# Performance work log

Measured on AMD Instinct MI355X. Metric: run time of the kernel, lower is better.

The kernel has to match this reference:

```python
import jax, jax.numpy as jnp
import numpy as np

EPS_LN = 1e-6


def _ln(x):
    m = jnp.mean(x, axis=-1, keepdims=True)
    v = jnp.mean((x - m) ** 2, axis=-1, keepdims=True)
    return (x - m) * jax.lax.rsqrt(v + EPS_LN)


def _rope(q, cos, sin):
    # q: [B,S,H,D]; cos/sin: [S, D//2]; rotate interleaved pairs
    q2 = q.reshape(q.shape[:-1] + (-1, 2))
    a, b = q2[..., 0], q2[..., 1]
    c = cos[None, :, None, :]
    s = sin[None, :, None, :]
    return jnp.stack([a * c - b * s, a * s + b * c], axis=-1).reshape(q.shape)


def _attn(q, k, v):
    # q:[B,Sq,H,D] k,v:[B,Sk,H,D] -> [B,Sq,H,D]; flash default scale 1/sqrt(D)
    D = q.shape[-1]
    scores = jnp.einsum('bqhd,bkhd->bhqk', q, k) / jnp.sqrt(jnp.asarray(D, q.dtype))
    p = jax.nn.softmax(scores, axis=-1)
    return jnp.einsum('bhqk,bkhd->bqhd', p, v)


def setup_inputs() -> dict:
    key = jax.random.key(0)
    C, H, S, T, B = 2048, 16, 1024, 256, 4
    Dh = C // H
    F = int(C * 4)
    L, Ly = B * S, B * T
    ks = jax.random.split(key, 24)

    def w(k, shape):
        return (jax.random.normal(k, shape, dtype=jnp.float32) * 0.02)

    # RoPE angle table: positions 0..S-1 with standard inverse frequencies
    inv_freq = 1.0 / (10000.0 ** (np.arange(0, Dh, 2, dtype=np.float32) / Dh))
    freqs = jnp.asarray(np.arange(S, dtype=np.float32)[:, None] * inv_freq[None, :])

    inp = {
        'x': jax.random.normal(ks[0], (L, C), dtype=jnp.float32),
        'y': jax.random.normal(ks[1], (Ly, C), dtype=jnp.float32),
        't': jax.random.normal(ks[2], (L, 6 * C), dtype=jnp.float32),
        'freqs': freqs,
        'scale_shift_table': jax.random.normal(ks[3], (6, C), dtype=jnp.float32) / (C ** 0.5),
        'Wq_s': w(ks[4], (C, C)), 'bq_s': jnp.zeros((C,), jnp.float32),
        'Wk_s': w(ks[5], (C, C)), 'bk_s': jnp.zeros((C,), jnp.float32),
        'Wv_s': w(ks[6], (C, C)), 'bv_s': jnp.zeros((C,), jnp.float32),
        'Wo_s': w(ks[7], (C, C)), 'bo_s': jnp.zeros((C,), jnp.float32),
        'Wq_c': w(ks[8], (C, C)), 'bq_c': jnp.zeros((C,), jnp.float32),
        'Wk_c': w(ks[9], (C, C)), 'bk_c': jnp.zeros((C,), jnp.float32),
        'Wv_c': w(ks[10], (C, C)), 'bv_c': jnp.zeros((C,), jnp.float32),
        'Wo_c': w(ks[11], (C, C)), 'bo_c': jnp.zeros((C,), jnp.float32),
        'W_fc1': w(ks[12], (F, C)), 'b_fc1': jnp.zeros((F,), jnp.float32),
        'W_fc2': w(ks[13], (C, F)), 'b_fc2': jnp.zeros((C,), jnp.float32),
        'seq_len': S,
        'txt_len': T,
    }
    return inp


def reference(x, y, t, freqs, scale_shift_table,
              Wq_s, bq_s, Wk_s, bk_s, Wv_s, bv_s, Wo_s, bo_s,
              Wq_c, bq_c, Wk_c, bk_c, Wv_c, bv_c, Wo_c, bo_c,
              W_fc1, b_fc1, W_fc2, b_fc2, seq_len, txt_len):
    L, C = x.shape
    Dh = 2 * freqs.shape[1]
    H = C // Dh
    B = L // seq_len
    cos, sin = jnp.cos(freqs), jnp.sin(freqs)

    # per-token AdaLN params (B here == total tokens in torch code)
    mods = scale_shift_table[None] + t.reshape(L, 6, C)
    shift_msa, scale_msa, gate_msa, shift_mlp, scale_mlp, gate_mlp = (
        mods[:, i, :] for i in range(6))

    # ---- self attention (AdaLN modulate + RoPE) ----
    xm = _ln(x) * (1.0 + scale_msa) + shift_msa
    q = (xm @ Wq_s.T + bq_s).reshape(B, seq_len, H, Dh)
    k = (xm @ Wk_s.T + bk_s).reshape(B, seq_len, H, Dh)
    v = (xm @ Wv_s.T + bv_s).reshape(B, seq_len, H, Dh)
    q = _rope(q, cos, sin)
    k = _rope(k, cos, sin)
    a = _attn(q, k, v).reshape(L, C)
    x = x + gate_msa * (a @ Wo_s.T + bo_s)

    # ---- cross attention (no norm/modulation/gate, no RoPE) ----
    q = (x @ Wq_c.T + bq_c).reshape(B, seq_len, H, Dh)
    k = (y @ Wk_c.T + bk_c).reshape(B, txt_len, H, Dh)
    v = (y @ Wv_c.T + bv_c).reshape(B, txt_len, H, Dh)
    a = _attn(q, k, v).reshape(L, C)
    x = x + (a @ Wo_c.T + bo_c)

    # ---- MLP with AdaLN modulate + gate ----
    xm = _ln(x) * (1.0 + scale_mlp) + shift_mlp
    h = jax.nn.gelu(xm @ W_fc1.T + b_fc1, approximate=True)
    x = x + gate_mlp * (h @ W_fc2.T + b_fc2)
    return x
```

## Files before the change

kernel.cpp:

```cpp
#include <hip/hip_runtime.h>
#include <stdint.h>

#define C_DIM 2048
#define H_NUM 16
#define DH    128
#define S_LEN 1024
#define T_LEN 256
#define B_SZ  4
#define L_ROWS 4096
#define LY_ROWS 1024
#define F_DIM 8192

typedef __attribute__((ext_vector_type(4))) float f32x4;
typedef __attribute__((ext_vector_type(8))) __bf16 bf16x8;
typedef __attribute__((ext_vector_type(4))) unsigned short us4;
typedef __attribute__((ext_vector_type(8))) unsigned short us8;
typedef unsigned short u16;

__device__ __forceinline__ u16 f2bf(float f) {
  union { float f; uint32_t u; } v; v.f = f;
  uint32_t r = v.u + 0x7FFFu + ((v.u >> 16) & 1u);
  return (u16)(r >> 16);
}
__device__ __forceinline__ float bf2f(u16 h) {
  union { uint32_t u; float f; } v; v.u = ((uint32_t)h) << 16;
  return v.f;
}

typedef __attribute__((address_space(1))) void gvoid;
typedef __attribute__((address_space(3))) void lvoid;
__device__ __forceinline__ void gl_lds16(const void* g, void* l) {
  __builtin_amdgcn_global_load_lds((gvoid*)g, (lvoid*)l, 16, 0, 0);
}

template<int N> __device__ __forceinline__ void wait_vmcnt() {
  if constexpr (N == 0) asm volatile("s_waitcnt vmcnt(0)" ::: "memory");
  else if constexpr (N == 4) asm volatile("s_waitcnt vmcnt(4)" ::: "memory");
  else if constexpr (N == 5) asm volatile("s_waitcnt vmcnt(5)" ::: "memory");
  else if constexpr (N == 6) asm volatile("s_waitcnt vmcnt(6)" ::: "memory");
}
__device__ __forceinline__ void barrier_raw() {
  asm volatile("s_barrier" ::: "memory");
}
__device__ __forceinline__ void lgkm0_pin() {
  asm volatile("s_waitcnt lgkmcnt(0)" ::: "memory");
  __builtin_amdgcn_sched_barrier(0);
}

__device__ __forceinline__ float gelu_fast(float val) {
  float z = 0.7978845608f * (val + 0.044715f * val * val * val);
  float e = __expf(2.f * z);
  float th = 1.f - 2.f / (e + 1.f);
  return 0.5f * val * (1.f + th);
}

__global__ void k_cvt(const float* __restrict__ src, u16* __restrict__ dst, int n) {
  int i = (blockIdx.x * blockDim.x + threadIdx.x) * 4;
  int stride = gridDim.x * blockDim.x * 4;
  for (; i < n; i += stride) {
    float4 v = *(const float4*)(src + i);
    us4 o;
    o[0] = f2bf(v.x); o[1] = f2bf(v.y); o[2] = f2bf(v.z); o[3] = f2bf(v.w);
    *(us4*)(dst + i) = o;
  }
}

__global__ void k_cvt8(const float* __restrict__ s0, const float* __restrict__ s1,
                       const float* __restrict__ s2, const float* __restrict__ s3,
                       const float* __restrict__ s4, const float* __restrict__ s5,
                       const float* __restrict__ s6, const float* __restrict__ s7,
                       u16* __restrict__ dst) {
  const int PER = C_DIM * C_DIM;
  int i = (blockIdx.x * blockDim.x + threadIdx.x) * 4;
  int stride = gridDim.x * blockDim.x * 4;
  int total = PER * 8;
  for (; i < total; i += stride) {
    int t = i >> 22;
    const float* s;
    switch (t) {
      case 0: s = s0; break; case 1: s = s1; break;
      case 2: s = s2; break; case 3: s = s3; break;
      case 4: s = s4; break; case 5: s = s5; break;
      case 6: s = s6; break; default: s = s7; break;
    }
    float4 v = *(const float4*)(s + (i & (PER - 1)));
    us4 o;
    o[0] = f2bf(v.x); o[1] = f2bf(v.y); o[2] = f2bf(v.z); o[3] = f2bf(v.w);
    *(us4*)(dst + i) = o;
  }
}

__global__ void k_cvt2(const float* __restrict__ s0, const float* __restrict__ s1,
                       u16* __restrict__ dst) {
  const int PER = F_DIM * C_DIM;
  int i = (blockIdx.x * blockDim.x + threadIdx.x) * 4;
  int stride = gridDim.x * blockDim.x * 4;
  int total = PER * 2;
  for (; i < total; i += stride) {
    const float* s = (i >> 24) ? s1 : s0;
    float4 v = *(const float4*)(s + (i & (PER - 1)));
    us4 o;
    o[0] = f2bf(v.x); o[1] = f2bf(v.y); o[2] = f2bf(v.z); o[3] = f2bf(v.w);
    *(us4*)(dst + i) = o;
  }
}

template<int INBF>
__global__ __launch_bounds__(256)
void k_modln(const void* __restrict__ xin, const float* __restrict__ t,
             const float* __restrict__ tab, u16* __restrict__ out,
             int scale_idx, int shift_idx) {
  int row = blockIdx.x;
  int tid = threadIdx.x;
  int c0 = tid * 8;
  float v[8];
  if constexpr (INBF) {
    us8 a = *(const us8*)((const u16*)xin + (size_t)row * C_DIM + c0);
#pragma unroll
    for (int j = 0; j < 8; ++j) v[j] = bf2f(a[j]);
  } else {
    const float* xr = (const float*)xin + (size_t)row * C_DIM;
    float4 a = *(const float4*)(xr + c0);
    float4 b = *(const float4*)(xr + c0 + 4);
    v[0] = a.x; v[1] = a.y; v[2] = a.z; v[3] = a.w;
    v[4] = b.x; v[5] = b.y; v[6] = b.z; v[7] = b.w;
  }
  float s = 0.f, ss = 0.f;
#pragma unroll
  for (int j = 0; j < 8; ++j) { s += v[j]; ss += v[j] * v[j]; }
#pragma unroll
  for (int m = 1; m < 64; m <<= 1) { s += __shfl_xor(s, m); ss += __shfl_xor(ss, m); }
  __shared__ float red[8];
  int wid = tid >> 6;
  if ((tid & 63) == 0) { red[wid * 2] = s; red[wid * 2 + 1] = ss; }
  __syncthreads();
  s  = red[0] + red[2] + red[4] + red[6];
  ss = red[1] + red[3] + red[5] + red[7];
  float mean = s * (1.f / C_DIM);
  float var  = ss * (1.f / C_DIM) - mean * mean;
  float rstd = rsqrtf(var + 1e-6f);
  const float* trow = t + (size_t)row * (6 * C_DIM);
  const float* tsc = trow + scale_idx * C_DIM + c0;
  const float* tsh = trow + shift_idx * C_DIM + c0;
  const float* gsc = tab + scale_idx * C_DIM + c0;
  const float* gsh = tab + shift_idx * C_DIM + c0;
  us8 o;
#pragma unroll
  for (int j = 0; j < 8; ++j) {
    float scv = 1.f + gsc[j] + tsc[j];
    float shv = gsh[j] + tsh[j];
    o[j] = f2bf((v[j] - mean) * rstd * scv + shv);
  }
  *(us8*)(out + (size_t)row * C_DIM + c0) = o;
}

template<int EPI>
__global__ __launch_bounds__(512, 2)
void k_gemm5(const u16* __restrict__ A, const u16* __restrict__ W,
             const float* __restrict__ bias0, const float* __restrict__ bias1,
             const float* __restrict__ bias2,
             u16* __restrict__ o0, u16* __restrict__ o1, u16* __restrict__ o2,
             int sec_shift, int out_ld,
             int M, int N, int K, int lda, int ldw, int nbx) {
  __shared__ __align__(16) u16 lds[65536];

  int tid = threadIdx.x;
  int nwg = gridDim.x;
  int q8 = nwg >> 3, r8 = nwg & 7;
  int xcd = blockIdx.x & 7, local = blockIdx.x >> 3;
  int wgid = (xcd < r8 ? xcd * (q8 + 1) : r8 * (q8 + 1) + (xcd - r8) * q8) + local;
  int bx = wgid % nbx, by = wgid / nbx;
  int m0 = by * 256, n0 = bx * 256;

  int wid = tid >> 6, lane = tid & 63;
  int wm = wid >> 2, wn = wid & 3;
  int lr = lane & 15, lg = lane >> 4;
  int xorslot = lr & 7;
  int bcol = (wn & 1) * 64;

  int srow = tid >> 3;
  int scol = ((tid ^ (tid >> 3)) & 7) * 8;

  auto stA = [&](int buf, int h, int kt) {
    u16* dst = lds + (buf * 2 + h) * 8192 + tid * 8;
#pragma unroll
    for (int call = 0; call < 2; ++call) {
      int grow = m0 + h * 128 + call * 64 + srow;
      gl_lds16(A + (size_t)grow * lda + kt * 64 + scol, dst + call * 4096);
    }
  };
  auto stB = [&](int buf, int h, int kt) {
    u16* dst = lds + 32768 + (buf * 2 + h) * 8192 + tid * 8;
#pragma unroll
    for (int call = 0; call < 2; ++call) {
      int grow = n0 + h * 128 + call * 64 + srow;
      gl_lds16(W + (size_t)grow * ldw + kt * 64 + scol, dst + call * 4096);
    }
  };

  f32x4 zero4 = {0.f, 0.f, 0.f, 0.f};
  f32x4 acc[8][4];
#pragma unroll
  for (int m = 0; m < 8; ++m)
#pragma unroll
    for (int n = 0; n < 4; ++n) acc[m][n] = zero4;

  int NT = K >> 6, NJ = NT >> 1;
  stA(0, 0, 0); stA(0, 1, 0); stB(0, 0, 0); stB(0, 1, 0);
  stB(1, 0, 1); stA(1, 0, 1);
  wait_vmcnt<4>();
  barrier_raw();

  for (int j = 0; j < NJ; ++j) {
    bool nlast = (j + 1 < NJ);
    int t1 = 2 * j + 1, t2 = 2 * j + 2, t3 = 2 * j + 3;
#pragma unroll
    for (int buf = 0; buf < 2; ++buf) {
      const u16* Ah = lds + (buf * 2 + wm) * 8192;
      const u16* Bh = lds + 32768 + (buf * 2 + (wn >> 1)) * 8192;
      bf16x8 aR[4][2], b0[2][2], b1[2][2];

#pragma unroll
      for (int m = 0; m < 4; ++m) {
        int r = m * 16 + lr;
#pragma unroll
        for (int kk = 0; kk < 2; ++kk)
          aR[m][kk] = *(const bf16x8*)(Ah + r * 64 + (((kk << 2) | lg) ^ xorslot) * 8);
      }
#pragma unroll
      for (int n = 0; n < 2; ++n) {
        int r = bcol + n * 16 + lr;
#pragma unroll
        for (int kk = 0; kk < 2; ++kk)
          b0[n][kk] = *(const bf16x8*)(Bh + r * 64 + (((kk << 2) | lg) ^ xorslot) * 8);
      }
      if (buf == 0) stA(1, 1, t1);
      else if (nlast) stA(0, 1, t2);
      barrier_raw();
      lgkm0_pin();
      __builtin_amdgcn_s_setprio(1);
#pragma unroll
      for (int kk = 0; kk < 2; ++kk)
#pragma unroll
        for (int m = 0; m < 4; ++m)
#pragma unroll
          for (int n = 0; n < 2; ++n)
            acc[m][n] = __builtin_amdgcn_mfma_f32_16x16x32_bf16(aR[m][kk], b0[n][kk], acc[m][n], 0, 0, 0);
      __builtin_amdgcn_s_setprio(0);
      barrier_raw();

#pragma unroll
      for (int n = 0; n < 2; ++n) {
        int r = bcol + 32 + n * 16 + lr;
#pragma unroll
        for (int kk = 0; kk < 2; ++kk)
          b1[n][kk] = *(const bf16x8*)(Bh + r * 64 + (((kk << 2) | lg) ^ xorslot) * 8);
      }
      if (buf == 0) stB(1, 1, t1);
      else if (nlast) stB(0, 1, t2);
      barrier_raw();
      lgkm0_pin();
      __builtin_amdgcn_s_setprio(1);
#pragma unroll
      for (int kk = 0; kk < 2; ++kk)
#pragma unroll
        for (int m = 0; m < 4; ++m)
#pragma unroll
          for (int n = 0; n < 2; ++n)
            acc[m][2 + n] = __builtin_amdgcn_mfma_f32_16x16x32_bf16(aR[m][kk], b1[n][kk], acc[m][2 + n], 0, 0, 0);
      __builtin_amdgcn_s_setprio(0);
      barrier_raw();

#pragma unroll
      for (int m = 0; m < 4; ++m) {
        int r = 64 + m * 16 + lr;
#pragma unroll
        for (int kk = 0; kk < 2; ++kk)
          aR[m][kk] = *(const bf16x8*)(Ah + r * 64 + (((kk << 2) | lg) ^ xorslot) * 8);
      }
      if (nlast) { if (buf == 0) stB(0, 0, t2); else stB(1, 0, t3); }
      barrier_raw();
      lgkm0_pin();
      __builtin_amdgcn_s_setprio(1);
#pragma unroll
      for (int kk = 0; kk < 2; ++kk)
#pragma unroll
        for (int m = 0; m < 4; ++m)
#pragma unroll
          for (int n = 0; n < 2; ++n)
            acc[4 + m][2 + n] = __builtin_amdgcn_mfma_f32_16x16x32_bf16(aR[m][kk], b1[n][kk], acc[4 + m][2 + n], 0, 0, 0);
      __builtin_amdgcn_s_setprio(0);
      barrier_raw();

      if (nlast) { if (buf == 0) stA(0, 0, t2); else stA(1, 0, t3); }
      barrier_raw();
      __builtin_amdgcn_s_setprio(1);
#pragma unroll
      for (int kk = 0; kk < 2; ++kk)
#pragma unroll
        for (int m = 0; m < 4; ++m)
#pragma unroll
          for (int n = 0; n < 2; ++n)
            acc[4 + m][n] = __builtin_amdgcn_mfma_f32_16x16x32_bf16(aR[m][kk], b0[n][kk], acc[4 + m][n], 0, 0, 0);
      __builtin_amdgcn_s_setprio(0);
      if (nlast) wait_vmcnt<4>(); else wait_vmcnt<0>();
      barrier_raw();
    }
  }

#pragma unroll
  for (int mf = 0; mf < 8; ++mf) {
    int row0 = m0 + wm * 128 + mf * 16 + lg * 4;
#pragma unroll
    for (int nf = 0; nf < 4; ++nf) {
      int col = n0 + wn * 64 + nf * 16 + lr;
      if constexpr (EPI == 0) {
        int sec = col >> sec_shift;
        const float* bp = sec == 0 ? bias0 : (sec == 1 ? bias1 : bias2);
        u16* op = sec == 0 ? o0 : (sec == 1 ? o1 : o2);
        int cs = col & ((1 << sec_shift) - 1);
        float bv = bp[cs];
#pragma unroll
        for (int r = 0; r < 4; ++r)
          op[(size_t)(row0 + r) * out_ld + cs] = f2bf(acc[mf][nf][r] + bv);
      } else {
        float bv = bias0[col];
#pragma unroll
        for (int r = 0; r < 4; ++r)
          o0[(size_t)(row0 + r) * out_ld + col] = f2bf(gelu_fast(acc[mf][nf][r] + bv));
      }
    }
  }
}

template<int BM, int EPI>
__global__ __launch_bounds__(512, 2)
void k_gemm3(const u16* __restrict__ A, const u16* __restrict__ W,
             const float* __restrict__ bias0, const float* __restrict__ bias1,
             const float* __restrict__ bias2,
             u16* __restrict__ o0, u16* __restrict__ o1, u16* __restrict__ o2,
             int sec_shift, int out_ld,
             float* __restrict__ outF, const float* __restrict__ resid,
             const float* __restrict__ gate_t, const float* __restrict__ gate_tab,
             int M, int N, int K, int lda, int ldw, int nbx) {
  constexpr int HTA = (BM / 2) * 64;
  constexpr int HTB = 128 * 64;
  constexpr int ACALLS = BM / 128;
  constexpr int QM = BM / 64;
  constexpr int MFR = BM / 32;
  constexpr int VMN = 4 + ACALLS;
  constexpr int BOFF = 4 * HTA;
  __shared__ __align__(16) u16 lds[BOFF + 4 * HTB];

  int tid = threadIdx.x;
  int nwg = gridDim.x;
  int q8 = nwg >> 3, r8 = nwg & 7;
  int xcd = blockIdx.x & 7, local = blockIdx.x >> 3;
  int wgid = (xcd < r8 ? xcd * (q8 + 1) : r8 * (q8 + 1) + (xcd - r8) * q8) + local;
  int bx = wgid % nbx, by = wgid / nbx;
  int m0 = by * BM, n0 = bx * 256;

  int wid = tid >> 6, lane = tid & 63;
  int wm = wid >> 2, wn = wid & 3;
  int lr = lane & 15, lg = lane >> 4;
  int xorslot = lr & 7;
  int bcol = (wn & 1) * 64;

  int srow = tid >> 3;
  int scol = ((tid ^ (tid >> 3)) & 7) * 8;

  auto stA = [&](int h, int kt2) {
    int pt = kt2 & 1;
    u16* dst = lds + (pt * 2 + h) * HTA + tid * 8;
#pragma unroll
    for (int call = 0; call < ACALLS; ++call) {
      int grow = m0 + h * (BM / 2) + call * 64 + srow;
      gl_lds16(A + (size_t)grow * lda + kt2 * 64 + scol, dst + call * 4096);
    }
  };
  auto stB = [&](int h, int kt2) {
    int pt = kt2 & 1;
    u16* dst = lds + BOFF + (pt * 2 + h) * HTB + tid * 8;
#pragma unroll
    for (int call = 0; call < 2; ++call) {
      int grow = n0 + h * 128 + call * 64 + srow;
      gl_lds16(W + (size_t)grow * ldw + kt2 * 64 + scol, dst + call * 4096);
    }
  };

  f32x4 zero4 = {0.f, 0.f, 0.f, 0.f};
  f32x4 acc[MFR][4];
#pragma unroll
  for (int m = 0; m < MFR; ++m)
#pragma unroll
    for (int n = 0; n < 4; ++n) acc[m][n] = zero4;

  int NT2 = K >> 6;
  stA(0, 0); stA(1, 0); stB(0, 0); stB(1, 0);
  stB(0, 1); stB(1, 1); stA(0, 1);
  wait_vmcnt<VMN>();
  barrier_raw();

  for (int kt = 0; kt < NT2; ++kt) {
    int p = kt & 1;
    const u16* Ah = lds + (p * 2 + wm) * HTA;
    const u16* Bh = lds + BOFF + (p * 2 + (wn >> 1)) * HTB;
    bf16x8 aR[QM][2], bR0[2][2], bR1[2][2];
    bool st1 = (kt + 1) < NT2, st2 = (kt + 2) < NT2;

#pragma unroll
    for (int m = 0; m < QM; ++m) {
      int r = m * 16 + lr;
#pragma unroll
      for (int kk = 0; kk < 2; ++kk)
        aR[m][kk] = *(const bf16x8*)(Ah + r * 64 + (((kk << 2) | lg) ^ xorslot) * 8);
    }
#pragma unroll
    for (int n = 0; n < 2; ++n) {
      int r = bcol + n * 16 + lr;
#pragma unroll
      for (int kk = 0; kk < 2; ++kk)
        bR0[n][kk] = *(const bf16x8*)(Bh + r * 64 + (((kk << 2) | lg) ^ xorslot) * 8);
    }
    if (st1) stA(1, kt + 1);
    lgkm0_pin();
    __builtin_amdgcn_s_setprio(1);
#pragma unroll
    for (int kk = 0; kk < 2; ++kk)
#pragma unroll
      for (int m = 0; m < QM; ++m)
#pragma unroll
        for (int n = 0; n < 2; ++n)
          acc[m][n] = __builtin_amdgcn_mfma_f32_16x16x32_bf16(aR[m][kk], bR0[n][kk], acc[m][n], 0, 0, 0);
    __builtin_amdgcn_s_setprio(0);
    barrier_raw();

#pragma unroll
    for (int n = 0; n < 2; ++n) {
      int r = bcol + 32 + n * 16 + lr;
#pragma unroll
      for (int kk = 0; kk < 2; ++kk)
        bR1[n][kk] = *(const bf16x8*)(Bh + r * 64 + (((kk << 2) | lg) ^ xorslot) * 8);
    }
    lgkm0_pin();
    __builtin_amdgcn_s_setprio(1);
#pragma unroll
    for (int kk = 0; kk < 2; ++kk)
#pragma unroll
      for (int m = 0; m < QM; ++m)
#pragma unroll
        for (int n = 0; n < 2; ++n)
          acc[m][2 + n] = __builtin_amdgcn_mfma_f32_16x16x32_bf16(aR[m][kk], bR1[n][kk], acc[m][2 + n], 0, 0, 0);
    __builtin_amdgcn_s_setprio(0);
    barrier_raw();

#pragma unroll
    for (int m = 0; m < QM; ++m) {
      int r = (BM / 4) + m * 16 + lr;
#pragma unroll
      for (int kk = 0; kk < 2; ++kk)
        aR[m][kk] = *(const bf16x8*)(Ah + r * 64 + (((kk << 2) | lg) ^ xorslot) * 8);
    }
    if (st2) { stB(0, kt + 2); stB(1, kt + 2); }
    lgkm0_pin();
    __builtin_amdgcn_s_setprio(1);
#pragma unroll
    for (int kk = 0; kk < 2; ++kk)
#pragma unroll
      for (int m = 0; m < QM; ++m)
#pragma unroll
        for (int n = 0; n < 2; ++n)
          acc[QM + m][2 + n] = __builtin_amdgcn_mfma_f32_16x16x32_bf16(aR[m][kk], bR1[n][kk], acc[QM + m][2 + n], 0, 0, 0);
    __builtin_amdgcn_s_setprio(0);
    barrier_raw();

    if (st2) stA(0, kt + 2);
    __builtin_amdgcn_s_setprio(1);
#pragma unroll
    for (int kk = 0; kk < 2; ++kk)
#pragma unroll
      for (int m = 0; m < QM; ++m)
#pragma unroll
        for (int n = 0; n < 2; ++n)
          acc[QM + m][n] = __builtin_amdgcn_mfma_f32_16x16x32_bf16(aR[m][kk], bR0[n][kk], acc[QM + m][n], 0, 0, 0);
    __builtin_amdgcn_s_setprio(0);
    if (st2) wait_vmcnt<VMN>(); else wait_vmcnt<0>();
    barrier_raw();
  }

#pragma unroll
  for (int mf = 0; mf < MFR; ++mf) {
    int row0 = m0 + wm * (BM / 2) + mf * 16 + lg * 4;
#pragma unroll
    for (int nf = 0; nf < 4; ++nf) {
      int col = n0 + wn * 64 + nf * 16 + lr;
      if constexpr (EPI == 0) {
        int sec = col >> sec_shift;
        const float* bp = sec == 0 ? bias0 : (sec == 1 ? bias1 : bias2);
        u16* op = sec == 0 ? o0 : (sec == 1 ? o1 : o2);
        int cs = col & ((1 << sec_shift) - 1);
        float bv = bp[cs];
#pragma unroll
        for (int r = 0; r < 4; ++r)
          op[(size_t)(row0 + r) * out_ld + cs] = f2bf(acc[mf][nf][r] + bv);
      } else if constexpr (EPI == 6) {
        float bv = bias0[col];
        float gt = gate_tab[col];
#pragma unroll
        for (int r = 0; r < 4; ++r) {
          int row = row0 + r;
          size_t idx = (size_t)row * N + col;
          float g = gt + gate_t[(size_t)row * (6 * C_DIM) + col];
          o0[idx] = f2bf(resid[idx] + g * (acc[mf][nf][r] + bv));
        }
      } else if constexpr (EPI == 7) {
        float bv = bias0[col];
#pragma unroll
        for (int r = 0; r < 4; ++r) {
          size_t idx = (size_t)(row0 + r) * N + col;
          o0[idx] = f2bf(bf2f(o0[idx]) + acc[mf][nf][r] + bv);
        }
      } else {
        float bv = bias0[col];
        float gt = gate_tab[col];
#pragma unroll
        for (int r = 0; r < 4; ++r) {
          int row = row0 + r;
          size_t idx = (size_t)row * N + col;
          float g = gt + gate_t[(size_t)row * (6 * C_DIM) + col];
          outF[idx] = bf2f(((const u16*)o1)[idx]) + g * (acc[mf][nf][r] + bv);
        }
      }
    }
  }
}

__global__ void k_rope(u16* __restrict__ q, u16* __restrict__ k,
                       const float* __restrict__ freqs) {
  int idx = blockIdx.x * blockDim.x + threadIdx.x;
  int total = L_ROWS * C_DIM / 8;
  for (; idx < total; idx += gridDim.x * blockDim.x) {
    int e = idx * 8;
    int row = e >> 11;
    int col = e & (C_DIM - 1);
    int s = row & (S_LEN - 1);
    int i0 = (col & (DH - 1)) >> 1;
    float4 fr = *(const float4*)(freqs + s * (DH / 2) + i0);
    float cs[4], sn[4];
    float fv[4] = {fr.x, fr.y, fr.z, fr.w};
#pragma unroll
    for (int j = 0; j < 4; ++j) __sincosf(fv[j], &sn[j], &cs[j]);
    us8 qa = *(us8*)(q + e);
    us8 ka = *(us8*)(k + e);
#pragma unroll
    for (int p = 0; p < 4; ++p) {
      float a = bf2f(qa[2 * p]), b = bf2f(qa[2 * p + 1]);
      qa[2 * p]     = f2bf(a * cs[p] - b * sn[p]);
      qa[2 * p + 1] = f2bf(a * sn[p] + b * cs[p]);
      float a2 = bf2f(ka[2 * p]), b2 = bf2f(ka[2 * p + 1]);
      ka[2 * p]     = f2bf(a2 * cs[p] - b2 * sn[p]);
      ka[2 * p + 1] = f2bf(a2 * sn[p] + b2 * cs[p]);
    }
    *(us8*)(q + e) = qa;
    *(us8*)(k + e) = ka;
  }
}

__global__ void k_transpose_v(const u16* __restrict__ v, u16* __restrict__ vt, int Lkv) {
  __shared__ u16 tile[32][33];
  int bh = blockIdx.x, b = bh >> 4, h = bh & 15;
  int k0 = blockIdx.y * 32, d0 = blockIdx.z * 32;
  int tx = threadIdx.x, ty = threadIdx.y;
  const u16* src = v + (size_t)(b * Lkv) * C_DIM + h * DH;
#pragma unroll
  for (int j = 0; j < 32; j += 8)
    tile[ty + j][tx] = src[(size_t)(k0 + ty + j) * C_DIM + d0 + tx];
  __syncthreads();
  u16* dst = vt + (size_t)bh * DH * Lkv;
#pragma unroll
  for (int j = 0; j < 32; j += 8)
    dst[(size_t)(d0 + ty + j) * Lkv + k0 + tx] = tile[tx][ty + j];
}

__global__ __launch_bounds__(256)
void k_flash(const u16* __restrict__ Q, const u16* __restrict__ K,
             const u16* __restrict__ Vt, u16* __restrict__ O,
             int Lq, int Lkv, float scale2) {
  __shared__ __align__(16) u16 lK[64 * 128];
  __shared__ __align__(16) u16 lV[128 * 64];
  __shared__ __align__(16) u16 lP[4][16 * 72];
  int bh = blockIdx.x, b = bh >> 4, h = bh & 15;
  int tid = threadIdx.x, wid = tid >> 6, lane = tid & 63;
  int lr = lane & 15, lg = lane >> 4;
  int q0 = blockIdx.y * 64 + wid * 16;
  const u16* Qb = Q + ((size_t)(b * Lq) + q0) * C_DIM + h * DH;
  const u16* Kb = K + (size_t)(b * Lkv) * C_DIM + h * DH;
  const u16* Vb = Vt + (size_t)bh * DH * Lkv;

  bf16x8 qf[4];
#pragma unroll
  for (int ks = 0; ks < 4; ++ks)
    qf[ks] = *(const bf16x8*)(Qb + (size_t)lr * C_DIM + ks * 32 + lg * 8);

  f32x4 zero4 = {0.f, 0.f, 0.f, 0.f};
  f32x4 o[8];
#pragma unroll
  for (int n = 0; n < 8; ++n) o[n] = zero4;
  float mrow[4] = {-3.0e38f, -3.0e38f, -3.0e38f, -3.0e38f};
  float lrow[4] = {0.f, 0.f, 0.f, 0.f};

  int nsteps = Lkv >> 6;
  for (int kt = 0; kt < nsteps; ++kt) {
#pragma unroll
    for (int i = 0; i < 4; ++i) {
      int flat = i * 4096 + tid * 16;
      int key = flat >> 8, inner = flat & 255;
      int ksrc = inner ^ ((key & 7) << 4);
      gl_lds16((const char*)Kb + ((size_t)(kt * 64 + key) * C_DIM) * 2 + ksrc, (char*)lK + flat);
      int d = flat >> 7, keyb = flat & 127;
      int vsrc = keyb ^ ((d & 7) << 4);
      gl_lds16((const char*)Vb + ((size_t)d * Lkv) * 2 + kt * 128 + vsrc, (char*)lV + flat);
    }
    __syncthreads();

    f32x4 sc[4];
#pragma unroll
    for (int c = 0; c < 4; ++c) sc[c] = zero4;
#pragma unroll
    for (int c = 0; c < 4; ++c) {
      int key = c * 16 + lr;
#pragma unroll
      for (int ks = 0; ks < 4; ++ks) {
        int off = (ks * 64 + lg * 16) ^ ((key & 7) << 4);
        bf16x8 kf = *(const bf16x8*)((const char*)lK + key * 256 + off);
        sc[c] = __builtin_amdgcn_mfma_f32_16x16x32_bf16(qf[ks], kf, sc[c], 0, 0, 0);
      }
    }
#pragma unroll
    for (int r = 0; r < 4; ++r) {
      float s0 = sc[0][r] * scale2, s1 = sc[1][r] * scale2;
      float s2 = sc[2][r] * scale2, s3 = sc[3][r] * scale2;
      float mx = fmaxf(fmaxf(s0, s1), fmaxf(s2, s3));
#pragma unroll
      for (int m = 1; m < 16; m <<= 1) mx = fmaxf(mx, __shfl_xor(mx, m));
      float mnew = fmaxf(mrow[r], mx);
      float alpha = exp2f(mrow[r] - mnew);
      mrow[r] = mnew;
      float p0 = exp2f(s0 - mnew);
      float p1 = exp2f(s1 - mnew);
      float p2 = exp2f(s2 - mnew);
      float p3 = exp2f(s3 - mnew);
      float psum = p0 + p1 + p2 + p3;
#pragma unroll
      for (int m = 1; m < 16; m <<= 1) psum += __shfl_xor(psum, m);
      lrow[r] = lrow[r] * alpha + psum;
#pragma unroll
      for (int n = 0; n < 8; ++n) o[n][r] *= alpha;
      u16* pr = lP[wid] + (4 * lg + r) * 72;
      pr[lr]      = f2bf(p0);
      pr[16 + lr] = f2bf(p1);
      pr[32 + lr] = f2bf(p2);
      pr[48 + lr] = f2bf(p3);
    }
    asm volatile("s_waitcnt lgkmcnt(0)" ::: "memory");
    __builtin_amdgcn_sched_barrier(0);
#pragma unroll
    for (int half = 0; half < 2; ++half) {
      bf16x8 pf = *(const bf16x8*)(lP[wid] + lr * 72 + half * 32 + lg * 8);
#pragma unroll
      for (int n = 0; n < 8; ++n) {
        int d = n * 16 + lr;
        int off = (half * 64 + lg * 16) ^ ((d & 7) << 4);
        bf16x8 vf = *(const bf16x8*)((const char*)lV + d * 128 + off);
        o[n] = __builtin_amdgcn_mfma_f32_16x16x32_bf16(pf, vf, o[n], 0, 0, 0);
      }
    }
    __syncthreads();
  }

  u16* Ob = O + ((size_t)(b * Lq) + q0) * C_DIM + h * DH;
#pragma unroll
  for (int n = 0; n < 8; ++n) {
    int d = n * 16 + lr;
#pragma unroll
    for (int r = 0; r < 4; ++r) {
      int qr = 4 * lg + r;
      Ob[(size_t)qr * C_DIM + d] = f2bf(o[n][r] / lrow[r]);
    }
  }
}

extern "C" void kernel_launch(void* const* d_in, const int* in_sizes, int n_in,
                              void* d_out, int out_size, void* d_ws, size_t ws_size,
                              hipStream_t stream) {
  const float* x     = (const float*)d_in[0];
  const float* y     = (const float*)d_in[1];
  const float* t     = (const float*)d_in[2];
  const float* freqs = (const float*)d_in[3];
  const float* tab   = (const float*)d_in[4];
  const float* Wq_s = (const float*)d_in[5];
  const float* bq_s = (const float*)d_in[6];
  const float* Wk_s = (const float*)d_in[7];
  const float* bk_s = (const float*)d_in[8];
  const float* Wv_s = (const float*)d_in[9];
  const float* bv_s = (const float*)d_in[10];
  const float* Wo_s = (const float*)d_in[11];
  const float* bo_s = (const float*)d_in[12];
  const float* Wq_c = (const float*)d_in[13];
  const float* bq_c = (const float*)d_in[14];
  const float* Wk_c = (const float*)d_in[15];
  const float* bk_c = (const float*)d_in[16];
  const float* Wv_c = (const float*)d_in[17];
  const float* bv_c = (const float*)d_in[18];
  const float* Wo_c = (const float*)d_in[19];
  const float* bo_c = (const float*)d_in[20];
  const float* W_fc1 = (const float*)d_in[21];
  const float* b_fc1 = (const float*)d_in[22];
  const float* W_fc2 = (const float*)d_in[23];
  const float* b_fc2 = (const float*)d_in[24];

  const size_t SZ_CC  = (size_t)C_DIM * C_DIM * 2;
  const size_t SZ_FC  = (size_t)F_DIM * C_DIM * 2;
  const size_t SZ_LC  = (size_t)L_ROWS * C_DIM * 2;
  const size_t SZ_YC  = (size_t)LY_ROWS * C_DIM * 2;
  char* ws = (char*)d_ws;
  size_t off = 0;
  u16* wq_s = (u16*)(ws + off); off += SZ_CC;
  u16* wk_s = (u16*)(ws + off); off += SZ_CC;
  u16* wv_s = (u16*)(ws + off); off += SZ_CC;
  u16* wo_s = (u16*)(ws + off); off += SZ_CC;
  u16* wq_c = (u16*)(ws + off); off += SZ_CC;
  u16* wk_c = (u16*)(ws + off); off += SZ_CC;
  u16* wv_c = (u16*)(ws + off); off += SZ_CC;
  u16* wo_c = (u16*)(ws + off); off += SZ_CC;
  u16* wfc1 = (u16*)(ws + off); off += SZ_FC;
  u16* wfc2 = (u16*)(ws + off); off += SZ_FC;
  u16* ybf  = (u16*)(ws + off); off += SZ_YC;
  u16* xm   = (u16*)(ws + off); off += SZ_LC;
  u16* qb   = (u16*)(ws + off); off += SZ_LC;
  u16* kb   = (u16*)(ws + off); off += SZ_LC;
  u16* vb   = (u16*)(ws + off); off += SZ_LC;
  u16* ao   = (u16*)(ws + off); off += SZ_LC;
  u16* hbuf = qb;
  u16* x1bf = (u16*)(ws + off); off += SZ_LC;
  u16* kc   = (u16*)(ws + off); off += SZ_YC;
  u16* vc   = (u16*)(ws + off); off += SZ_YC;
  u16* vt   = (u16*)(ws + off); off += SZ_LC;
  u16* vtc  = (u16*)(ws + off); off += SZ_YC;
  if (ws_size < off) return;

  k_cvt8<<<4096, 256, 0, stream>>>(Wq_s, Wk_s, Wv_s, Wo_s, Wq_c, Wk_c, Wv_c, Wo_c, wq_s);
  k_cvt2<<<4096, 256, 0, stream>>>(W_fc1, W_fc2, wfc1);
  k_cvt<<<2048, 256, 0, stream>>>(y, ybf, LY_ROWS * C_DIM);

  const float ascale2 = 0.08838834764831845f * 1.44269504f;

  k_modln<0><<<L_ROWS, 256, 0, stream>>>(x, t, tab, xm, 1, 0);
  k_gemm3<128, 0><<<32 * 24, 512, 0, stream>>>(
      xm, wq_s, bq_s, bk_s, bv_s, qb, kb, vb, 11, C_DIM,
      nullptr, nullptr, nullptr, nullptr, L_ROWS, 6144, C_DIM, C_DIM, C_DIM, 24);
  k_rope<<<2048, 256, 0, stream>>>(qb, kb, freqs);
  k_transpose_v<<<dim3(B_SZ * H_NUM, S_LEN / 32, DH / 32), dim3(32, 8), 0, stream>>>(vb, vt, S_LEN);
  k_flash<<<dim3(B_SZ * H_NUM, S_LEN / 64), 256, 0, stream>>>(qb, kb, vt, ao, S_LEN, S_LEN, ascale2);
  k_gemm3<128, 6><<<32 * 8, 512, 0, stream>>>(
      ao, wo_s, bo_s, nullptr, nullptr, x1bf, nullptr, nullptr, 30, C_DIM,
      nullptr, x, t + 2 * C_DIM, tab + 2 * C_DIM, L_ROWS, C_DIM, C_DIM, C_DIM, C_DIM, 8);
  k_gemm3<128, 0><<<32 * 8, 512, 0, stream>>>(
      x1bf, wq_c, bq_c, nullptr, nullptr, qb, nullptr, nullptr, 30, C_DIM,
      nullptr, nullptr, nullptr, nullptr, L_ROWS, C_DIM, C_DIM, C_DIM, C_DIM, 8);
  k_gemm3<128, 0><<<8 * 16, 512, 0, stream>>>(
      ybf, wk_c, bk_c, bv_c, bv_c, kc, vc, vc, 11, C_DIM,
      nullptr, nullptr, nullptr, nullptr, LY_ROWS, 4096, C_DIM, C_DIM, C_DIM, 16);
  k_transpose_v<<<dim3(B_SZ * H_NUM, T_LEN / 32, DH / 32), dim3(32, 8), 0, stream>>>(vc, vtc, T_LEN);
  k_flash<<<dim3(B_SZ * H_NUM, S_LEN / 64), 256, 0, stream>>>(qb, kc, vtc, ao, S_LEN, T_LEN, ascale2);
  k_gemm3<128, 7><<<32 * 8, 512, 0, stream>>>(
      ao, wo_c, bo_c, nullptr, nullptr, x1bf, nullptr, nullptr, 30, C_DIM,
      nullptr, nullptr, nullptr, nullptr, L_ROWS, C_DIM, C_DIM, C_DIM, C_DIM, 8);
  k_modln<1><<<L_ROWS, 256, 0, stream>>>(x1bf, t, tab, xm, 4, 3);
  k_gemm5<1><<<16 * 32, 512, 0, stream>>>(
      xm, wfc1, b_fc1, nullptr, nullptr, hbuf, nullptr, nullptr, 30, F_DIM,
      L_ROWS, F_DIM, C_DIM, C_DIM, C_DIM, 32);
  k_gemm3<128, 8><<<32 * 8, 512, 0, stream>>>(
      hbuf, wfc2, b_fc2, nullptr, nullptr, nullptr, x1bf, nullptr, 30, C_DIM,
      (float*)d_out, nullptr, t + 5 * C_DIM, tab + 5 * C_DIM, L_ROWS, C_DIM, F_DIM, F_DIM, F_DIM, 8);
}
```

Measured before the change: 843.0 us.

## Fuse RoPE and V transpose into QKV projection GEMM epilogues

The self-attention QKV GEMM epilogue now applies RoPE to Q and K, pairing even and odd columns with a lane shuffle and computing sincos from the freqs table. It also writes V directly in the transposed per-head layout that flash attention expects. The cross-attention KV GEMM likewise writes V transposed, so the separate rope and transpose kernels and their extra global round trips are gone. The cost is heavier epilogues with per-element sincos and strided, poorly coalesced transposed stores. An unused multi-output path was also dropped from the FC1 GEMM.

Measured after the change: 835.2 us. No clear change (-0.9%).

```diff
diff --git a/kernel.cpp b/kernel.cpp
--- a/kernel.cpp
+++ b/kernel.cpp
@@ -157,10 +157,8 @@
 template<int EPI>
 __global__ __launch_bounds__(512, 2)
 void k_gemm5(const u16* __restrict__ A, const u16* __restrict__ W,
-             const float* __restrict__ bias0, const float* __restrict__ bias1,
-             const float* __restrict__ bias2,
-             u16* __restrict__ o0, u16* __restrict__ o1, u16* __restrict__ o2,
-             int sec_shift, int out_ld,
+             const float* __restrict__ bias0,
+             u16* __restrict__ o0, int out_ld,
              int M, int N, int K, int lda, int ldw, int nbx) {
   __shared__ __align__(16) u16 lds[65536];
 
@@ -314,21 +312,10 @@
 #pragma unroll
     for (int nf = 0; nf < 4; ++nf) {
       int col = n0 + wn * 64 + nf * 16 + lr;
-      if constexpr (EPI == 0) {
-        int sec = col >> sec_shift;
-        const float* bp = sec == 0 ? bias0 : (sec == 1 ? bias1 : bias2);
-        u16* op = sec == 0 ? o0 : (sec == 1 ? o1 : o2);
-        int cs = col & ((1 << sec_shift) - 1);
-        float bv = bp[cs];
-#pragma unroll
-        for (int r = 0; r < 4; ++r)
-          op[(size_t)(row0 + r) * out_ld + cs] = f2bf(acc[mf][nf][r] + bv);
-      } else {
-        float bv = bias0[col];
-#pragma unroll
-        for (int r = 0; r < 4; ++r)
-          o0[(size_t)(row0 + r) * out_ld + col] = f2bf(gelu_fast(acc[mf][nf][r] + bv));
-      }
+      float bv = bias0[col];
+#pragma unroll
+      for (int r = 0; r < 4; ++r)
+        o0[(size_t)(row0 + r) * out_ld + col] = f2bf(gelu_fast(acc[mf][nf][r] + bv));
     }
   }
 }
@@ -520,7 +507,7 @@
           size_t idx = (size_t)(row0 + r) * N + col;
           o0[idx] = f2bf(bf2f(o0[idx]) + acc[mf][nf][r] + bv);
         }
-      } else {
+      } else if constexpr (EPI == 8) {
         float bv = bias0[col];
         float gt = gate_tab[col];
 #pragma unroll
@@ -530,56 +517,57 @@
           float g = gt + gate_t[(size_t)row * (6 * C_DIM) + col];
           outF[idx] = bf2f(((const u16*)o1)[idx]) + g * (acc[mf][nf][r] + bv);
         }
+      } else if constexpr (EPI == 9) {
+        int sec = col >> 11;
+        int cs = col & 2047;
+        const float* bp = sec == 0 ? bias0 : (sec == 1 ? bias1 : bias2);
+        float bv = bp[cs];
+        if (sec < 2) {
+          u16* op = sec == 0 ? o0 : o1;
+          int i0 = (cs & (DH - 1)) >> 1;
+          bool even = (cs & 1) == 0;
+#pragma unroll
+          for (int r = 0; r < 4; ++r) {
+            float val = acc[mf][nf][r] + bv;
+            float pv = __shfl_xor(val, 1);
+            int sr = (row0 + r) & (S_LEN - 1);
+            float ang = gate_t[sr * (DH / 2) + i0];
+            float sn, csn;
+            __sincosf(ang, &sn, &csn);
+            float outv = even ? (val * csn - pv * sn) : (pv * sn + val * csn);
+            op[(size_t)(row0 + r) * out_ld + cs] = f2bf(outv);
+          }
+        } else {
+          int h = cs >> 7, d = cs & (DH - 1);
+#pragma unroll
+          for (int r = 0; r < 4; ++r) {
+            int row = row0 + r;
+            int b = row >> 10, kv = row & (S_LEN - 1);
+            o2[(((size_t)(b * H_NUM + h) * DH + d) << 10) + kv] =
+                f2bf(acc[mf][nf][r] + bv);
+          }
+        }
+      } else {
+        int sec = col >> 11;
+        int cs = col & 2047;
+        float bv = (sec == 0 ? bias0 : bias1)[cs];
+        if (sec == 0) {
+#pragma unroll
+          for (int r = 0; r < 4; ++r)
+            o0[(size_t)(row0 + r) * out_ld + cs] = f2bf(acc[mf][nf][r] + bv);
+        } else {
+          int h = cs >> 7, d = cs & (DH - 1);
+#pragma unroll
+          for (int r = 0; r < 4; ++r) {
+            int row = row0 + r;
+            int b = row >> 8, kv = row & (T_LEN - 1);
+            o1[(((size_t)(b * H_NUM + h) * DH + d) << 8) + kv] =
+                f2bf(acc[mf][nf][r] + bv);
+          }
+        }
       }
     }
   }
-}
-
-__global__ void k_rope(u16* __restrict__ q, u16* __restrict__ k,
-                       const float* __restrict__ freqs) {
-  int idx = blockIdx.x * blockDim.x + threadIdx.x;
-  int total = L_ROWS * C_DIM / 8;
-  for (; idx < total; idx += gridDim.x * blockDim.x) {
-    int e = idx * 8;
-    int row = e >> 11;
-    int col = e & (C_DIM - 1);
-    int s = row & (S_LEN - 1);
-    int i0 = (col & (DH - 1)) >> 1;
-    float4 fr = *(const float4*)(freqs + s * (DH / 2) + i0);
-    float cs[4], sn[4];
-    float fv[4] = {fr.x, fr.y, fr.z, fr.w};
-#pragma unroll
-    for (int j = 0; j < 4; ++j) __sincosf(fv[j], &sn[j], &cs[j]);
-    us8 qa = *(us8*)(q + e);
-    us8 ka = *(us8*)(k + e);
-#pragma unroll
-    for (int p = 0; p < 4; ++p) {
-      float a = bf2f(qa[2 * p]), b = bf2f(qa[2 * p + 1]);
-      qa[2 * p]     = f2bf(a * cs[p] - b * sn[p]);
-      qa[2 * p + 1] = f2bf(a * sn[p] + b * cs[p]);
-      float a2 = bf2f(ka[2 * p]), b2 = bf2f(ka[2 * p + 1]);
-      ka[2 * p]     = f2bf(a2 * cs[p] - b2 * sn[p]);
-      ka[2 * p + 1] = f2bf(a2 * sn[p] + b2 * cs[p]);
-    }
-    *(us8*)(q + e) = qa;
-    *(us8*)(k + e) = ka;
-  }
-}
-
-__global__ void k_transpose_v(const u16* __restrict__ v, u16* __restrict__ vt, int Lkv) {
-  __shared__ u16 tile[32][33];
-  int bh = blockIdx.x, b = bh >> 4, h = bh & 15;
-  int k0 = blockIdx.y * 32, d0 = blockIdx.z * 32;
-  int tx = threadIdx.x, ty = threadIdx.y;
-  const u16* src = v + (size_t)(b * Lkv) * C_DIM + h * DH;
-#pragma unroll
-  for (int j = 0; j < 32; j += 8)
-    tile[ty + j][tx] = src[(size_t)(k0 + ty + j) * C_DIM + d0 + tx];
-  __syncthreads();
-  u16* dst = vt + (size_t)bh * DH * Lkv;
-#pragma unroll
-  for (int j = 0; j < 32; j += 8)
-    dst[(size_t)(d0 + ty + j) * Lkv + k0 + tx] = tile[tx][ty + j];
 }
 
 __global__ __launch_bounds__(256)
@@ -748,6 +736,7 @@
   u16* vt   = (u16*)(ws + off); off += SZ_LC;
   u16* vtc  = (u16*)(ws + off); off += SZ_YC;
   if (ws_size < off) return;
+  (void)vb; (void)vc;
 
   k_cvt8<<<4096, 256, 0, stream>>>(Wq_s, Wk_s, Wv_s, Wo_s, Wq_c, Wk_c, Wv_c, Wo_c, wq_s);
   k_cvt2<<<4096, 256, 0, stream>>>(W_fc1, W_fc2, wfc1);
@@ -756,11 +745,9 @@
   const float ascale2 = 0.08838834764831845f * 1.44269504f;
 
   k_modln<0><<<L_ROWS, 256, 0, stream>>>(x, t, tab, xm, 1, 0);
-  k_gemm3<128, 0><<<32 * 24, 512, 0, stream>>>(
-      xm, wq_s, bq_s, bk_s, bv_s, qb, kb, vb, 11, C_DIM,
-      nullptr, nullptr, nullptr, nullptr, L_ROWS, 6144, C_DIM, C_DIM, C_DIM, 24);
-  k_rope<<<2048, 256, 0, stream>>>(qb, kb, freqs);
-  k_transpose_v<<<dim3(B_SZ * H_NUM, S_LEN / 32, DH / 32), dim3(32, 8), 0, stream>>>(vb, vt, S_LEN);
+  k_gemm3<128, 9><<<32 * 24, 512, 0, stream>>>(
+      xm, wq_s, bq_s, bk_s, bv_s, qb, kb, vt, 11, C_DIM,
+      nullptr, nullptr, freqs, nullptr, L_ROWS, 6144, C_DIM, C_DIM, C_DIM, 24);
   k_flash<<<dim3(B_SZ * H_NUM, S_LEN / 64), 256, 0, stream>>>(qb, kb, vt, ao, S_LEN, S_LEN, ascale2);
   k_gemm3<128, 6><<<32 * 8, 512, 0, stream>>>(
       ao, wo_s, bo_s, nullptr, nullptr, x1bf, nullptr, nullptr, 30, C_DIM,
@@ -768,18 +755,16 @@
   k_gemm3<128, 0><<<32 * 8, 512, 0, stream>>>(
       x1bf, wq_c, bq_c, nullptr, nullptr, qb, nullptr, nullptr, 30, C_DIM,
       nullptr, nullptr, nullptr, nullptr, L_ROWS, C_DIM, C_DIM, C_DIM, C_DIM, 8);
-  k_gemm3<128, 0><<<8 * 16, 512, 0, stream>>>(
-      ybf, wk_c, bk_c, bv_c, bv_c, kc, vc, vc, 11, C_DIM,
+  k_gemm3<128, 10><<<8 * 16, 512, 0, stream>>>(
+      ybf, wk_c, bk_c, bv_c, nullptr, kc, vtc, nullptr, 11, C_DIM,
       nullptr, nullptr, nullptr, nullptr, LY_ROWS, 4096, C_DIM, C_DIM, C_DIM, 16);
-  k_transpose_v<<<dim3(B_SZ * H_NUM, T_LEN / 32, DH / 32), dim3(32, 8), 0, stream>>>(vc, vtc, T_LEN);
   k_flash<<<dim3(B_SZ * H_NUM, S_LEN / 64), 256, 0, stream>>>(qb, kc, vtc, ao, S_LEN, T_LEN, ascale2);
   k_gemm3<128, 7><<<32 * 8, 512, 0, stream>>>(
       ao, wo_c, bo_c, nullptr, nullptr, x1bf, nullptr, nullptr, 30, C_DIM,
       nullptr, nullptr, nullptr, nullptr, L_ROWS, C_DIM, C_DIM, C_DIM, C_DIM, 8);
   k_modln<1><<<L_ROWS, 256, 0, stream>>>(x1bf, t, tab, xm, 4, 3);
   k_gemm5<1><<<16 * 32, 512, 0, stream>>>(
-      xm, wfc1, b_fc1, nullptr, nullptr, hbuf, nullptr, nullptr, 30, F_DIM,
-      L_ROWS, F_DIM, C_DIM, C_DIM, C_DIM, 32);
+      xm, wfc1, b_fc1, hbuf, F_DIM, L_ROWS, F_DIM, C_DIM, C_DIM, C_DIM, 32);
   k_gemm3<128, 8><<<32 * 8, 512, 0, stream>>>(
       hbuf, wfc2, b_fc2, nullptr, nullptr, nullptr, x1bf, nullptr, 30, C_DIM,
       (float*)d_out, nullptr, t + 5 * C_DIM, tab + 5 * C_DIM, L_ROWS, C_DIM, F_DIM, F_DIM, F_DIM, 8);
```
